# Performance work log

Measured on AMD Instinct MI355X. Metric: run time of the kernel, lower is better.

Reference implementation:

```python
import jax, jax.numpy as jnp
import numpy as np

V, E, H, W, L = 30000, 300, 512, 20, 512
EPS = 1e-8


def _lstm_dir(x, Wih, Whh):
    # x: [L, E]; PyTorch gate order i, f, g, o; bias=False
    Hh = Whh.shape[1]
    def step(carry, xt):
        h, c = carry
        g = Wih @ xt + Whh @ h
        i, f, gg, o = jnp.split(g, 4)
        c = jax.nn.sigmoid(f) * c + jax.nn.sigmoid(i) * jnp.tanh(gg)
        h = jax.nn.sigmoid(o) * jnp.tanh(c)
        return (h, c), h
    init = (jnp.zeros(Hh, x.dtype), jnp.zeros(Hh, x.dtype))
    _, hs = jax.lax.scan(step, init, x)
    return hs  # [L, H]


def _bilstm(x, Wih_f, Whh_f, Wih_b, Whh_b):
    hf = _lstm_dir(x, Wih_f, Whh_f)
    hb = _lstm_dir(x[::-1], Wih_b, Whh_b)[::-1]
    return jnp.concatenate([hf, hb], axis=-1)  # [L, 2H]


def _wcos_rows(a, b, w):
    # a,b: [L,H] (b may be broadcast of a single vector); w: [W,H] -> [L,W]
    A = a[:, None, :] * w[None]                       # [L,W,H]
    B = jnp.broadcast_to(b, a.shape)[:, None, :] * w[None]
    num = jnp.sum(A * B, axis=-1)
    na = jnp.maximum(jnp.linalg.norm(A, axis=-1), EPS)
    nb = jnp.maximum(jnp.linalg.norm(B, axis=-1), EPS)
    return num / (na * nb)


def _wcos_pair_max(a, b, w):
    # fused pairwise weighted cosine + max over q2: never builds [L1,L2,W,H]
    A = a[:, None, :] * w[None]                       # [L1,W,H]
    B = b[:, None, :] * w[None]                       # [L2,W,H]
    num = jnp.einsum('ikh,jkh->ijk', A, B)            # [L1,L2,W]
    na = jnp.maximum(jnp.linalg.norm(A, axis=-1), EPS)  # [L1,W]
    nb = jnp.maximum(jnp.linalg.norm(B, axis=-1), EPS)  # [L2,W]
    return jnp.max(num / (na[:, None, :] * nb[None, :, :]), axis=1)  # [L1,W]


def _cos_pair(a, b):
    num = a @ b.T                                     # [L1,L2]
    na = jnp.maximum(jnp.linalg.norm(a, axis=-1), EPS)
    nb = jnp.maximum(jnp.linalg.norm(b, axis=-1), EPS)
    return num / (na[:, None] * nb[None, :])


def _model(emb, q1_Wih_f, q1_Whh_f, q1_Wih_b, q1_Whh_b,
           q2_Wih_f, q2_Whh_f, q2_Wih_b, q2_Whh_b,
           W1, W2, W3, W4, W5, W6, q1_ids, q2_ids, l1, l2):
    Hh = W1.shape[1]
    x1 = emb[q1_ids[0, :l1]]                          # [L1,E]
    x2 = emb[q2_ids[0, :l2]]
    q1_outs = _bilstm(x1, q1_Wih_f, q1_Whh_f, q1_Wih_b, q1_Whh_b)
    q2_outs = _bilstm(x2, q2_Wih_f, q2_Whh_f, q2_Wih_b, q2_Whh_b)
    q1p, q1n = q1_outs[:, :Hh], q1_outs[:, Hh:]
    q2p, q2n = q2_outs[:, :Hh], q2_outs[:, Hh:]
    # full matching (vs q2 tail fwd / head bwd)
    m_pos_full = _wcos_rows(q1p, q2p[-1], W1)
    m_neg_full = _wcos_rows(q1n, q2n[0], W2)
    # max-pool matching over all q2 positions
    m_pos_max = _wcos_pair_max(q1p, q2p, W3)
    m_neg_max = _wcos_pair_max(q1n, q2n, W4)
    # attentive matching (cosine attention, mean-by-alpha)
    alpha_pos = _cos_pair(q1p, q2p)                   # [L1,L2]
    q2_pos_att = (alpha_pos @ q2p) / jnp.sum(alpha_pos, axis=1, keepdims=True)
    m_pos_atten = _wcos_rows(q1p, q2_pos_att, W5)
    alpha_neg = _cos_pair(q1n, q2n)
    q2_neg_att = (alpha_neg @ q2n) / jnp.sum(alpha_neg, axis=1, keepdims=True)
    m_neg_atten = _wcos_rows(q1n, q2_neg_att, W5)     # source uses W_5 here (not W_6), kept faithful
    return jnp.stack([m_pos_full, m_neg_full, m_pos_max,
                      m_neg_max, m_pos_atten, m_neg_atten])  # [6,L1,W]


def setup_inputs() -> dict:
    key = jax.random.key(0)
    ks = jax.random.split(key, 20)
    def n(k, shape, s=1.0):
        return jax.random.normal(k, shape, jnp.float32) * s
    return {
        'q1_inputs': jax.random.randint(ks[0], (1, L), 0, V),
        'q2_inputs': jax.random.randint(ks[1], (1, L), 0, V),
        'q1_lens': L,
        'q2_lens': L,
        'emb': n(ks[2], (V, E), 0.1),
        'q1_Wih_f': n(ks[3], (4 * H, E), 0.05), 'q1_Whh_f': n(ks[4], (4 * H, H), 0.05),
        'q1_Wih_b': n(ks[5], (4 * H, E), 0.05), 'q1_Whh_b': n(ks[6], (4 * H, H), 0.05),
        'q2_Wih_f': n(ks[7], (4 * H, E), 0.05), 'q2_Whh_f': n(ks[8], (4 * H, H), 0.05),
        'q2_Wih_b': n(ks[9], (4 * H, E), 0.05), 'q2_Whh_b': n(ks[10], (4 * H, H), 0.05),
        'W1': n(ks[11], (W, H)), 'W2': n(ks[12], (W, H)), 'W3': n(ks[13], (W, H)),
        'W4': n(ks[14], (W, H)), 'W5': n(ks[15], (W, H)), 'W6': n(ks[16], (W, H)),
    }


def reference(q1_inputs, q2_inputs, q1_lens, q2_lens, emb,
              q1_Wih_f, q1_Whh_f, q1_Wih_b, q1_Whh_b,
              q2_Wih_f, q2_Whh_f, q2_Wih_b, q2_Whh_b,
              W1, W2, W3, W4, W5, W6):
    return _model(emb, q1_Wih_f, q1_Whh_f, q1_Wih_b, q1_Whh_b,
                  q2_Wih_f, q2_Whh_f, q2_Wih_b, q2_Whh_b,
                  W1, W2, W3, W4, W5, W6,
                  q1_inputs, q2_inputs, q1_lens, q2_lens)
```

## Files before the change

kernel.cpp:

```cpp
#include <hip/hip_runtime.h>
#include <hip/hip_bf16.h>
#include <math.h>

#define LQ 512
#define HH 512
#define EE 300
#define WW 20
#define G4 2048
#define EPSF 1e-8f
#define RB 32
#define JPB 16

typedef __hip_bfloat16 bf16;
typedef unsigned long long u64;
typedef unsigned int u32;

__device__ __forceinline__ float fast_sigmoid(float x){
  x = fminf(fmaxf(x, -30.f), 30.f);
  return 1.f/(1.f + __expf(-x));
}
__device__ __forceinline__ float fast_tanh(float x){
  x = fminf(fmaxf(x, -15.f), 15.f);
  float e = __expf(2.f*x);
  return (e - 1.f)/(e + 1.f);
}

#define OFF_GIN   0
#define OFF_ALPHA 0
#define OFF_ATT   524288
#define OFF_NRM   1048576
#define OFF_NP    1089536
#define OFF_PMP   1179648
#define OFF_HS    (4*LQ*G4)
#define OFF_HPUB  (OFF_HS + 4*LQ*HH)
#define WS_NEEDED ((OFF_HPUB + 2*4*LQ*HH) * 4ULL)

__global__ __launch_bounds__(256) void k_sentinel(float* __restrict__ outp, float code)
{
  const int i = blockIdx.x*256 + threadIdx.x;
  if (i < 3072) outp[i] = code;
}

__global__ __launch_bounds__(256) void k_gather_gemm(
    const float* __restrict__ emb, const int* __restrict__ q1_ids, const int* __restrict__ q2_ids,
    const float* __restrict__ wih0, const float* __restrict__ wih1,
    const float* __restrict__ wih2, const float* __restrict__ wih3,
    float* __restrict__ gin)
{
  const int g = blockIdx.z;
  const int* ids = (g < 2) ? q1_ids : q2_ids;
  const float* wih = (g==0)?wih0:(g==1)?wih1:(g==2)?wih2:wih3;
  __shared__ __align__(16) float As[16][68];
  __shared__ __align__(16) float Bs[16][68];
  __shared__ int rowid[64];
  const int tid = threadIdx.x;
  const int tx = tid & 15, ty = tid >> 4;
  const int m0 = blockIdx.y*64, n0 = blockIdx.x*64;
  if (tid < 64) rowid[tid] = ids[m0 + tid];
  __syncthreads();
  float acc[4][4] = {};
  for (int k0 = 0; k0 < EE; k0 += 16) {
    for (int idx = tid; idx < 1024; idx += 256) {
      int r = idx >> 4, kk = idx & 15;
      int k = k0 + kk;
      As[kk][r] = (k < EE) ? emb[(size_t)rowid[r]*EE + k] : 0.f;
      Bs[kk][r] = (k < EE) ? wih[(size_t)(n0+r)*EE + k] : 0.f;
    }
    __syncthreads();
    #pragma unroll
    for (int kk=0;kk<16;kk++){
      float4 a = *reinterpret_cast<const float4*>(&As[kk][ty*4]);
      float4 b = *reinterpret_cast<const float4*>(&Bs[kk][tx*4]);
      acc[0][0]=fmaf(a.x,b.x,acc[0][0]); acc[0][1]=fmaf(a.x,b.y,acc[0][1]);
      acc[0][2]=fmaf(a.x,b.z,acc[0][2]); acc[0][3]=fmaf(a.x,b.w,acc[0][3]);
      acc[1][0]=fmaf(a.y,b.x,acc[1][0]); acc[1][1]=fmaf(a.y,b.y,acc[1][1]);
      acc[1][2]=fmaf(a.y,b.z,acc[1][2]); acc[1][3]=fmaf(a.y,b.w,acc[1][3]);
      acc[2][0]=fmaf(a.z,b.x,acc[2][0]); acc[2][1]=fmaf(a.z,b.y,acc[2][1]);
      acc[2][2]=fmaf(a.z,b.z,acc[2][2]); acc[2][3]=fmaf(a.z,b.w,acc[2][3]);
      acc[3][0]=fmaf(a.w,b.x,acc[3][0]); acc[3][1]=fmaf(a.w,b.y,acc[3][1]);
      acc[3][2]=fmaf(a.w,b.z,acc[3][2]); acc[3][3]=fmaf(a.w,b.w,acc[3][3]);
    }
    __syncthreads();
  }
  float* outp = gin + (size_t)g*LQ*G4;
  #pragma unroll
  for (int u=0;u<4;u++)
    #pragma unroll
    for (int v=0;v<4;v++)
      outp[(size_t)(m0+ty*4+u)*G4 + n0+tx*4+v] = acc[u][v];
}

__global__ __launch_bounds__(512)
__attribute__((amdgpu_waves_per_eu(1,2)))
void k_lstm(
    const float* __restrict__ whh0, const float* __restrict__ whh1,
    const float* __restrict__ whh2, const float* __restrict__ whh3,
    const float* __restrict__ gin, float* __restrict__ hs, u64* __restrict__ hpub)
{
  const int g = (blockIdx.x >> 1) & 3;
  const int b = ((blockIdx.x >> 3) << 1) | (blockIdx.x & 1);
  const float* whh = (g==0)?whh0:(g==1)?whh1:(g==2)?whh2:whh3;
  const int tid = threadIdx.x;
  const int row_local = tid >> 3;
  const int chunk = tid & 7;
  const int gate = row_local >> 4;
  const int jj = row_local & 15;
  const int grow = gate*HH + b*JPB + jj;
  const int rot = chunk;

  const float4* wv4 = reinterpret_cast<const float4*>(whh + (size_t)grow*HH + chunk*64);
  float4 w0  = wv4[(0  + rot) & 15];
  float4 w1  = wv4[(1  + rot) & 15];
  float4 w2  = wv4[(2  + rot) & 15];
  float4 w3  = wv4[(3  + rot) & 15];
  float4 w4  = wv4[(4  + rot) & 15];
  float4 w5  = wv4[(5  + rot) & 15];
  float4 w6  = wv4[(6  + rot) & 15];
  float4 w7  = wv4[(7  + rot) & 15];
  float4 w8  = wv4[(8  + rot) & 15];
  float4 w9  = wv4[(9  + rot) & 15];
  float4 w10 = wv4[(10 + rot) & 15];
  float4 w11 = wv4[(11 + rot) & 15];
  float4 w12 = wv4[(12 + rot) & 15];
  float4 w13 = wv4[(13 + rot) & 15];
  float4 w14 = wv4[(14 + rot) & 15];
  float4 w15 = wv4[(15 + rot) & 15];

  __shared__ __align__(16) float h_lds[HH];
  __shared__ float gdot[64];

  const float* ginp = gin + (size_t)g*LQ*G4;
  float* hsg = hs + (size_t)g*LQ*HH;
  u64* hpg = hpub + (size_t)g*LQ*HH;
  const bool fwd = ((g & 1) == 0);

  float pg_cur = 0.f, pg_nxt = 0.f, creg = 0.f;
  if (tid < 64) {
    const int sidx0 = fwd ? 0 : (LQ-1);
    pg_cur = ginp[(size_t)sidx0*G4 + (size_t)(tid>>4)*HH + b*JPB + (tid&15)];
  }

  for (int s=0; s<LQ; ++s) {
    const int sidx = fwd ? s : (LQ-1-s);
    if (s == 0) {
      h_lds[tid] = 0.f;
      __syncthreads();
    } else {
      const int hidx = fwd ? (s-1) : (LQ-s);
      const u64 want = (u64)(u32)(hidx + 1);
      const u64* hp = hpg + (size_t)hidx*HH + tid;
      u64 v = __hip_atomic_load(hp, __ATOMIC_RELAXED, __HIP_MEMORY_SCOPE_AGENT);
      while ((v >> 32) != want) {
        v = __hip_atomic_load(hp, __ATOMIC_RELAXED, __HIP_MEMORY_SCOPE_AGENT);
      }
      h_lds[tid] = __uint_as_float((u32)v);
      __syncthreads();
    }
    float p0=0.f, p1=0.f, p2=0.f, p3=0.f;
    {
      const float4* hld4 = reinterpret_cast<const float4*>(h_lds) + (chunk << 4);
      #define MSTEP(q, pp) { float4 hh = hld4[((q)+rot)&15]; \
        pp = fmaf(w##q.x, hh.x, pp); pp = fmaf(w##q.y, hh.y, pp); \
        pp = fmaf(w##q.z, hh.z, pp); pp = fmaf(w##q.w, hh.w, pp); }
      MSTEP(0,p0)  MSTEP(1,p1)  MSTEP(2,p2)  MSTEP(3,p3)
      MSTEP(4,p0)  MSTEP(5,p1)  MSTEP(6,p2)  MSTEP(7,p3)
      MSTEP(8,p0)  MSTEP(9,p1)  MSTEP(10,p2) MSTEP(11,p3)
      MSTEP(12,p0) MSTEP(13,p1) MSTEP(14,p2) MSTEP(15,p3)
      #undef MSTEP
    }
    if (tid < 64) {
      const int snx = (s+1 < LQ) ? (s+1) : s;
      const int sidxn = fwd ? snx : (LQ-1-snx);
      pg_nxt = ginp[(size_t)sidxn*G4 + (size_t)(tid>>4)*HH + b*JPB + (tid&15)];
    }
    float partial = (p0 + p1) + (p2 + p3);
    partial += __shfl_xor(partial, 1);
    partial += __shfl_xor(partial, 2);
    partial += __shfl_xor(partial, 4);
    if (chunk == 0) gdot[row_local] = partial;
    __syncthreads();
    if (tid < 64) {
      float x = gdot[tid] + pg_cur;
      const int gt = tid >> 4;
      float t = (gt == 2) ? 2.f*x : x;
      t = fminf(fmaxf(t, -30.f), 30.f);
      float sg = 1.f/(1.f + __expf(-t));
      float y = (gt == 2) ? 2.f*sg - 1.f : sg;
      float vf = __shfl_down(y, 16);
      float vg = __shfl_down(y, 32);
      float vo = __shfl_down(y, 48);
      if (tid < 16) {
        float c = vf*creg + y*vg;
        creg = c;
        float tc = fminf(fmaxf(2.f*c, -30.f), 30.f);
        float th = 2.f/(1.f + __expf(-tc)) - 1.f;
        float h = vo*th;
        const int j = b*JPB + tid;
        u64 pack = ((u64)(u32)(sidx + 1) << 32) | (u64)__float_as_uint(h);
        __hip_atomic_store(hpg + (size_t)sidx*HH + j, pack,
                           __ATOMIC_RELAXED, __HIP_MEMORY_SCOPE_AGENT);
        hsg[(size_t)sidx*HH + j] = h;
      }
      pg_cur = pg_nxt;
    }
  }
}

__global__ __launch_bounds__(256) void k_norms(
    const float* __restrict__ hs, const float* __restrict__ W3, const float* __restrict__ W4,
    float* __restrict__ nrm, float* __restrict__ np_)
{
  const int l = blockIdx.x;
  const int which = blockIdx.y;
  const int hsidx = (which==0)?0:(which==1)?2:(which==2)?1:3;
  const float* P = hs + (size_t)hsidx*LQ*HH + (size_t)l*HH;
  const float* Wt = (which < 2) ? W3 : W4;
  const int tid = threadIdx.x;
  const int w = tid >> 6, ln = tid & 63;
  __shared__ float p[HH];
  p[tid] = P[tid]; p[tid+256] = P[tid+256];
  __syncthreads();
  if (w == 0) {
    float v = 0.f;
    #pragma unroll
    for (int q=0;q<8;q++){ float x = p[ln+64*q]; v = fmaf(x,x,v); }
    #pragma unroll
    for (int o=32;o>0;o>>=1) v += __shfl_xor(v,o);
    if (ln==0) np_[which*LQ + l] = fmaxf(sqrtf(v), EPSF);
  }
  for (int k=w; k<WW; k+=4){
    const float* wk = Wt + (size_t)k*HH;
    float v = 0.f;
    #pragma unroll
    for (int q=0;q<8;q++){
      int e = ln + 64*q;
      float a = p[e]*wk[e];
      v = fmaf(a,a,v);
    }
    #pragma unroll
    for (int o=32;o>0;o>>=1) v += __shfl_xor(v,o);
    if (ln==0) nrm[(size_t)which*LQ*WW + (size_t)l*WW + k] = fmaxf(sqrtf(v), EPSF);
  }
}

__global__ __launch_bounds__(256) void k_alpha(
    const float* __restrict__ hs, const float* __restrict__ np_, float* __restrict__ alpha)
{
  const int z = blockIdx.z;
  const float* A = hs + (size_t)(z?1:0)*LQ*HH;
  const float* B = hs + (size_t)(z?3:2)*LQ*HH;
  const float* nai = np_ + (z?2:0)*LQ;
  const float* nbj = np_ + (z?3:1)*LQ;
  float* outp = alpha + (size_t)z*LQ*LQ;
  __shared__ __align__(16) float As[16][68], Bs[16][68];
  const int tid = threadIdx.x;
  const int tx = tid & 15, ty = tid >> 4;
  const int i0 = blockIdx.y*64, j0 = blockIdx.x*64;
  float acc[4][4] = {};
  for (int k0=0;k0<HH;k0+=16){
    for (int idx=tid; idx<1024; idx+=256){
      int r = idx>>4, kk = idx&15;
      As[kk][r] = A[(size_t)(i0+r)*HH + k0+kk];
      Bs[kk][r] = B[(size_t)(j0+r)*HH + k0+kk];
    }
    __syncthreads();
    #pragma unroll
    for (int kk=0;kk<16;kk++){
      float4 a = *reinterpret_cast<const float4*>(&As[kk][ty*4]);
      float4 b = *reinterpret_cast<const float4*>(&Bs[kk][tx*4]);
      acc[0][0]=fmaf(a.x,b.x,acc[0][0]); acc[0][1]=fmaf(a.x,b.y,acc[0][1]);
      acc[0][2]=fmaf(a.x,b.z,acc[0][2]); acc[0][3]=fmaf(a.x,b.w,acc[0][3]);
      acc[1][0]=fmaf(a.y,b.x,acc[1][0]); acc[1][1]=fmaf(a.y,b.y,acc[1][1]);
      acc[1][2]=fmaf(a.y,b.z,acc[1][2]); acc[1][3]=fmaf(a.y,b.w,acc[1][3]);
      acc[2][0]=fmaf(a.z,b.x,acc[2][0]); acc[2][1]=fmaf(a.z,b.y,acc[2][1]);
      acc[2][2]=fmaf(a.z,b.z,acc[2][2]); acc[2][3]=fmaf(a.z,b.w,acc[2][3]);
      acc[3][0]=fmaf(a.w,b.x,acc[3][0]); acc[3][1]=fmaf(a.w,b.y,acc[3][1]);
      acc[3][2]=fmaf(a.w,b.z,acc[3][2]); acc[3][3]=fmaf(a.w,b.w,acc[3][3]);
    }
    __syncthreads();
  }
  #pragma unroll
  for (int u=0;u<4;u++){
    float ina = 1.f/nai[i0+ty*4+u];
    #pragma unroll
    for (int v=0;v<4;v++)
      outp[(size_t)(i0+ty*4+u)*LQ + j0+tx*4+v] = acc[u][v]*ina/nbj[j0+tx*4+v];
  }
}

__global__ __launch_bounds__(256) void k_att(
    const float* __restrict__ alpha, const float* __restrict__ hs,
    float* __restrict__ att)
{
  const int z = blockIdx.z;
  const float* A = alpha + (size_t)z*LQ*LQ;
  const float* B = hs + (size_t)(z?3:2)*LQ*HH;
  float* outp = att + (size_t)z*LQ*HH;
  __shared__ __align__(16) float As[16][68], Bs[16][68];
  const int tid = threadIdx.x;
  const int tx = tid & 15, ty = tid >> 4;
  const int i0 = blockIdx.y*64, h0 = blockIdx.x*64;
  float acc[4][4] = {};
  float rsum[4] = {};
  for (int j0=0;j0<LQ;j0+=16){
    for (int idx=tid; idx<1024; idx+=256){
      int r = idx>>4, kk = idx&15;
      As[kk][r] = A[(size_t)(i0+r)*LQ + j0+kk];
    }
    for (int idx=tid; idx<1024; idx+=256){
      int jjr = idx>>6, hh = idx&63;
      Bs[jjr][hh] = B[(size_t)(j0+jjr)*HH + h0+hh];
    }
    __syncthreads();
    #pragma unroll
    for (int kk=0;kk<16;kk++){
      float4 a = *reinterpret_cast<const float4*>(&As[kk][ty*4]);
      float4 b = *reinterpret_cast<const float4*>(&Bs[kk][tx*4]);
      rsum[0]+=a.x; rsum[1]+=a.y; rsum[2]+=a.z; rsum[3]+=a.w;
      acc[0][0]=fmaf(a.x,b.x,acc[0][0]); acc[0][1]=fmaf(a.x,b.y,acc[0][1]);
      acc[0][2]=fmaf(a.x,b.z,acc[0][2]); acc[0][3]=fmaf(a.x,b.w,acc[0][3]);
      acc[1][0]=fmaf(a.y,b.x,acc[1][0]); acc[1][1]=fmaf(a.y,b.y,acc[1][1]);
      acc[1][2]=fmaf(a.y,b.z,acc[1][2]); acc[1][3]=fmaf(a.y,b.w,acc[1][3]);
      acc[2][0]=fmaf(a.z,b.x,acc[2][0]); acc[2][1]=fmaf(a.z,b.y,acc[2][1]);
      acc[2][2]=fmaf(a.z,b.z,acc[2][2]); acc[2][3]=fmaf(a.z,b.w,acc[2][3]);
      acc[3][0]=fmaf(a.w,b.x,acc[3][0]); acc[3][1]=fmaf(a.w,b.y,acc[3][1]);
      acc[3][2]=fmaf(a.w,b.z,acc[3][2]); acc[3][3]=fmaf(a.w,b.w,acc[3][3]);
    }
    __syncthreads();
  }
  #pragma unroll
  for (int u=0;u<4;u++){
    float inv = 1.f/rsum[u];
    #pragma unroll
    for (int v=0;v<4;v++)
      outp[(size_t)(i0+ty*4+u)*HH + h0+tx*4+v] = acc[u][v]*inv;
  }
}

__global__ __launch_bounds__(256) void k_wcos(
    const float* __restrict__ hs, const float* __restrict__ att,
    const float* __restrict__ W1, const float* __restrict__ W2, const float* __restrict__ W5,
    float* __restrict__ outp)
{
  const int l = blockIdx.x;
  const int which = blockIdx.y;
  const int tid = threadIdx.x;
  const float* a; const float* c; const float* Wt; int m;
  switch (which) {
    case 0:  a = hs + (size_t)0*LQ*HH + (size_t)l*HH; c = hs + (size_t)2*LQ*HH + (size_t)(LQ-1)*HH; Wt = W1; m = 0; break;
    case 1:  a = hs + (size_t)1*LQ*HH + (size_t)l*HH; c = hs + (size_t)3*LQ*HH;                     Wt = W2; m = 1; break;
    case 2:  a = hs + (size_t)0*LQ*HH + (size_t)l*HH; c = att + (size_t)0*LQ*HH + (size_t)l*HH;     Wt = W5; m = 4; break;
    default: a = hs + (size_t)1*LQ*HH + (size_t)l*HH; c = att + (size_t)1*LQ*HH + (size_t)l*HH;     Wt = W5; m = 5; break;
  }
  __shared__ float av[HH], cv[HH];
  const int w = tid >> 6, ln = tid & 63;
  av[tid]=a[tid]; av[tid+256]=a[tid+256];
  cv[tid]=c[tid]; cv[tid+256]=c[tid+256];
  __syncthreads();
  for (int k=w; k<WW; k+=4){
    const float* wk = Wt + (size_t)k*HH;
    float num=0.f, na=0.f, nc=0.f;
    #pragma unroll
    for (int q=0;q<8;q++){
      int e = ln + 64*q;
      float w1 = wk[e];
      float aw = av[e]*w1;
      float cw = cv[e]*w1;
      num = fmaf(aw,cw,num);
      na  = fmaf(aw,aw,na);
      nc  = fmaf(cw,cw,nc);
    }
    #pragma unroll
    for (int o=32;o>0;o>>=1){
      num += __shfl_xor(num,o);
      na  += __shfl_xor(na,o);
      nc  += __shfl_xor(nc,o);
    }
    if (ln==0){
      float d = fmaxf(sqrtf(na),EPSF)*fmaxf(sqrtf(nc),EPSF);
      outp[((size_t)m*LQ + l)*WW + k] = num/d;
    }
  }
}

__global__ __launch_bounds__(256) void k_pairmax(
    const float* __restrict__ hs, const float* __restrict__ W3, const float* __restrict__ W4,
    const float* __restrict__ nrm, float* __restrict__ pm_part)
{
  const int it = blockIdx.x;
  const int jt = blockIdx.y;
  const int z  = blockIdx.z;
  const int mm = z >> 1, kh = z & 1;
  const int k0 = kh*10;
  const float* A = hs + (size_t)(mm?1:0)*LQ*HH;
  const float* B = hs + (size_t)(mm?3:2)*LQ*HH;
  const float* Wt = mm ? W4 : W3;
  const float* nb = nrm + (size_t)(mm?3:1)*LQ*WW;
  const int tid = threadIdx.x;
  const int tx = tid & 31;
  const int ty = tid >> 5;
  const int i0 = it*64;
  const int j  = jt*32 + tx;

  __shared__ __align__(16) float As[64][128];
  __shared__ __align__(16) float Bs[32][132];
  __shared__ __align__(16) float Ws[10][128];

  float acc[8][10];
  #pragma unroll
  for (int r=0;r<8;r++)
    #pragma unroll
    for (int q=0;q<10;q++) acc[r][q]=0.f;

  for (int hc=0; hc<4; ++hc){
    const int hbase = hc*128;
    for (int idx=tid; idx<2048; idx+=256){
      int row = idx >> 5, c4 = idx & 31;
      *reinterpret_cast<float4*>(&As[row][c4*4]) =
        *reinterpret_cast<const float4*>(&A[(size_t)(i0+row)*HH + hbase + c4*4]);
    }
    for (int idx=tid; idx<1024; idx+=256){
      int row = idx >> 5, c4 = idx & 31;
      *reinterpret_cast<float4*>(&Bs[row][c4*4]) =
        *reinterpret_cast<const float4*>(&B[(size_t)(jt*32+row)*HH + hbase + c4*4]);
    }
    for (int idx=tid; idx<1280; idx+=256){
      int kk = idx >> 7, cc = idx & 127;
      float wv = Wt[(size_t)(k0+kk)*HH + hbase + cc];
      Ws[kk][cc] = wv*wv;
    }
    __syncthreads();
    #pragma unroll 2
    for (int h4=0; h4<32; ++h4){
      float4 b = *reinterpret_cast<const float4*>(&Bs[tx][h4*4]);
      float4 sa[8];
      #pragma unroll
      for (int r=0;r<8;r++){
        float4 a = *reinterpret_cast<const float4*>(&As[ty*8+r][h4*4]);
        sa[r].x = a.x*b.x; sa[r].y = a.y*b.y;
        sa[r].z = a.z*b.z; sa[r].w = a.w*b.w;
      }
      #pragma unroll
      for (int q=0;q<10;q++){
        float4 w = *reinterpret_cast<const float4*>(&Ws[q][h4*4]);
        #pragma unroll
        for (int r=0;r<8;r++){
          acc[r][q] = fmaf(sa[r].x, w.x, acc[r][q]);
          acc[r][q] = fmaf(sa[r].y, w.y, acc[r][q]);
          acc[r][q] = fmaf(sa[r].z, w.z, acc[r][q]);
          acc[r][q] = fmaf(sa[r].w, w.w, acc[r][q]);
        }
      }
    }
    __syncthreads();
  }

  float nbv[10];
  #pragma unroll
  for (int q=0;q<10;q++) nbv[q] = 1.f / nb[(size_t)j*WW + k0 + q];
  #pragma unroll
  for (int r=0;r<8;r++){
    #pragma unroll
    for (int q=0;q<10;q++){
      float v = acc[r][q] * nbv[q];
      #pragma unroll
      for (int o=1;o<32;o<<=1) v = fmaxf(v, __shfl_xor(v, o, 32));
      if (tx==0)
        pm_part[((((size_t)z*8 + it)*16 + jt)*64 + (ty*8+r))*10 + q] = v;
    }
  }
}

__global__ __launch_bounds__(256) void k_pmfin(
    const float* __restrict__ pm_part, const float* __restrict__ nrm,
    float* __restrict__ outp)
{
  const int idx = blockIdx.x*256 + threadIdx.x;
  if (idx >= 2*LQ*WW) return;
  const int mm = idx / (LQ*WW);
  const int rem = idx - mm*LQ*WW;
  const int i = rem / WW, k = rem % WW;
  const int it = i >> 6, il = i & 63;
  const int kh = k / 10, kl = k % 10;
  const int z = mm*2 + kh;
  float v = -3.4e38f;
  #pragma unroll
  for (int jt=0; jt<16; ++jt)
    v = fmaxf(v, pm_part[((((size_t)z*8 + it)*16 + jt)*64 + il)*10 + kl]);
  const float* na = nrm + (size_t)(mm?2:0)*LQ*WW;
  outp[((size_t)(mm+2)*LQ + i)*WW + k] = v / na[(size_t)i*WW + k];
}

extern "C" void kernel_launch(void* const* d_in, const int* in_sizes, int n_in,
                              void* d_out, int out_size, void* d_ws, size_t ws_size,
                              hipStream_t stream)
{
  float* outp = (float*)d_out;

  float code = 0.f;
  if (n_in != 19)                    code = 101.f;
  else if (in_sizes[0]  != 512)      code = 102.f;
  else if (in_sizes[4]  != 9000000)  code = 104.f;
  else if (in_sizes[6]  != 1048576)  code = 106.f;
  else if (out_size     != 61440)    code = 108.f;
  else if (ws_size      < WS_NEEDED) code = 109.f;
  if (code != 0.f) {
    k_sentinel<<<12, 256, 0, stream>>>(outp, code);
    return;
  }

  const int* q1_ids = (const int*)d_in[0];
  const int* q2_ids = (const int*)d_in[1];
  const float* emb      = (const float*)d_in[4];
  const float* q1_wih_f = (const float*)d_in[5];
  const float* q1_whh_f = (const float*)d_in[6];
  const float* q1_wih_b = (const float*)d_in[7];
  const float* q1_whh_b = (const float*)d_in[8];
  const float* q2_wih_f = (const float*)d_in[9];
  const float* q2_whh_f = (const float*)d_in[10];
  const float* q2_wih_b = (const float*)d_in[11];
  const float* q2_whh_b = (const float*)d_in[12];
  const float* W1 = (const float*)d_in[13];
  const float* W2 = (const float*)d_in[14];
  const float* W3 = (const float*)d_in[15];
  const float* W4 = (const float*)d_in[16];
  const float* W5 = (const float*)d_in[17];
  float* ws = (float*)d_ws;

  float* gin   = ws + OFF_GIN;
  float* hsv   = ws + OFF_HS;
  u64*   hpub  = (u64*)(ws + OFF_HPUB);
  float* alpha = ws + OFF_ALPHA;
  float* att   = ws + OFF_ATT;
  float* nrm   = ws + OFF_NRM;
  float* np_   = ws + OFF_NP;
  float* pmp   = ws + OFF_PMP;

  k_gather_gemm<<<dim3(32,8,4), 256, 0, stream>>>(emb, q1_ids, q2_ids,
      q1_wih_f, q1_wih_b, q2_wih_f, q2_wih_b, gin);
  k_lstm<<<dim3(4*RB), 512, 0, stream>>>(q1_whh_f, q1_whh_b, q2_whh_f, q2_whh_b,
      gin, hsv, hpub);
  k_norms<<<dim3(LQ,4), 256, 0, stream>>>(hsv, W3, W4, nrm, np_);
  k_alpha<<<dim3(8,8,2), 256, 0, stream>>>(hsv, np_, alpha);
  k_att<<<dim3(8,8,2), 256, 0, stream>>>(alpha, hsv, att);
  k_wcos<<<dim3(LQ,4), 256, 0, stream>>>(hsv, att, W1, W2, W5, outp);
  k_pairmax<<<dim3(8,16,4), 256, 0, stream>>>(hsv, W3, W4, nrm, pmp);
  k_pmfin<<<dim3(80), 256, 0, stream>>>(pmp, nrm, outp);
}
```

Measured before the change: 1.225 ms.

## Fuse input-projection GEMM into LSTM kernel with tile-ready flags for overlap

Merges the gather+input-GEMM and the persistent LSTM recurrence into one launch. Extra blocks compute 128x128 GEMM tiles and publish a magic tag per tile, and LSTM blocks spin on the tag covering the timesteps they are about to consume. This lets the recurrence start before the whole projection finishes and drops a kernel boundary. The GEMM tile is also enlarged to 128x128 with vectorized stores. Tags are never reset, so a stale TAG_MAGIC from a previous call could let LSTM blocks read gin before it is rewritten. The design also relies on all 384 blocks being co-resident to avoid deadlock.

Result: slower. 1.515 ms (+23.7%).

```diff
diff --git a/kernel.cpp b/kernel.cpp
--- a/kernel.cpp
+++ b/kernel.cpp
@@ -10,20 +10,11 @@
 #define EPSF 1e-8f
 #define RB 32
 #define JPB 16
+#define TAG_MAGIC 0x7E57A11Bu
 
 typedef __hip_bfloat16 bf16;
 typedef unsigned long long u64;
 typedef unsigned int u32;
-
-__device__ __forceinline__ float fast_sigmoid(float x){
-  x = fminf(fmaxf(x, -30.f), 30.f);
-  return 1.f/(1.f + __expf(-x));
-}
-__device__ __forceinline__ float fast_tanh(float x){
-  x = fminf(fmaxf(x, -15.f), 15.f);
-  float e = __expf(2.f*x);
-  return (e - 1.f)/(e + 1.f);
-}
 
 #define OFF_GIN   0
 #define OFF_ALPHA 0
@@ -33,7 +24,13 @@
 #define OFF_PMP   1179648
 #define OFF_HS    (4*LQ*G4)
 #define OFF_HPUB  (OFF_HS + 4*LQ*HH)
-#define WS_NEEDED ((OFF_HPUB + 2*4*LQ*HH) * 4ULL)
+#define OFF_TAG   (OFF_HPUB + 2*4*LQ*HH)
+#define WS_NEEDED ((OFF_TAG + 1024) * 4ULL)
+
+__device__ __forceinline__ float load_f32_agent(const float* p){
+  u32 v = __hip_atomic_load((const u32*)p, __ATOMIC_RELAXED, __HIP_MEMORY_SCOPE_AGENT);
+  return __uint_as_float(v);
+}
 
 __global__ __launch_bounds__(256) void k_sentinel(float* __restrict__ outp, float code)
 {
@@ -41,72 +38,83 @@
   if (i < 3072) outp[i] = code;
 }
 
-__global__ __launch_bounds__(256) void k_gather_gemm(
+__global__ __launch_bounds__(512)
+__attribute__((amdgpu_waves_per_eu(1,2)))
+void k_fusedgl(
     const float* __restrict__ emb, const int* __restrict__ q1_ids, const int* __restrict__ q2_ids,
     const float* __restrict__ wih0, const float* __restrict__ wih1,
     const float* __restrict__ wih2, const float* __restrict__ wih3,
-    float* __restrict__ gin)
-{
-  const int g = blockIdx.z;
-  const int* ids = (g < 2) ? q1_ids : q2_ids;
-  const float* wih = (g==0)?wih0:(g==1)?wih1:(g==2)?wih2:wih3;
-  __shared__ __align__(16) float As[16][68];
-  __shared__ __align__(16) float Bs[16][68];
-  __shared__ int rowid[64];
-  const int tid = threadIdx.x;
-  const int tx = tid & 15, ty = tid >> 4;
-  const int m0 = blockIdx.y*64, n0 = blockIdx.x*64;
-  if (tid < 64) rowid[tid] = ids[m0 + tid];
-  __syncthreads();
-  float acc[4][4] = {};
-  for (int k0 = 0; k0 < EE; k0 += 16) {
-    for (int idx = tid; idx < 1024; idx += 256) {
-      int r = idx >> 4, kk = idx & 15;
-      int k = k0 + kk;
-      As[kk][r] = (k < EE) ? emb[(size_t)rowid[r]*EE + k] : 0.f;
-      Bs[kk][r] = (k < EE) ? wih[(size_t)(n0+r)*EE + k] : 0.f;
-    }
-    __syncthreads();
-    #pragma unroll
-    for (int kk=0;kk<16;kk++){
-      float4 a = *reinterpret_cast<const float4*>(&As[kk][ty*4]);
-      float4 b = *reinterpret_cast<const float4*>(&Bs[kk][tx*4]);
-      acc[0][0]=fmaf(a.x,b.x,acc[0][0]); acc[0][1]=fmaf(a.x,b.y,acc[0][1]);
-      acc[0][2]=fmaf(a.x,b.z,acc[0][2]); acc[0][3]=fmaf(a.x,b.w,acc[0][3]);
-      acc[1][0]=fmaf(a.y,b.x,acc[1][0]); acc[1][1]=fmaf(a.y,b.y,acc[1][1]);
-      acc[1][2]=fmaf(a.y,b.z,acc[1][2]); acc[1][3]=fmaf(a.y,b.w,acc[1][3]);
-      acc[2][0]=fmaf(a.z,b.x,acc[2][0]); acc[2][1]=fmaf(a.z,b.y,acc[2][1]);
-      acc[2][2]=fmaf(a.z,b.z,acc[2][2]); acc[2][3]=fmaf(a.z,b.w,acc[2][3]);
-      acc[3][0]=fmaf(a.w,b.x,acc[3][0]); acc[3][1]=fmaf(a.w,b.y,acc[3][1]);
-      acc[3][2]=fmaf(a.w,b.z,acc[3][2]); acc[3][3]=fmaf(a.w,b.w,acc[3][3]);
-    }
-    __syncthreads();
-  }
-  float* outp = gin + (size_t)g*LQ*G4;
-  #pragma unroll
-  for (int u=0;u<4;u++)
-    #pragma unroll
-    for (int v=0;v<4;v++)
-      outp[(size_t)(m0+ty*4+u)*G4 + n0+tx*4+v] = acc[u][v];
-}
-
-__global__ __launch_bounds__(512)
-__attribute__((amdgpu_waves_per_eu(1,2)))
-void k_lstm(
     const float* __restrict__ whh0, const float* __restrict__ whh1,
     const float* __restrict__ whh2, const float* __restrict__ whh3,
-    const float* __restrict__ gin, float* __restrict__ hs, u64* __restrict__ hpub)
-{
+    float* __restrict__ gin, float* __restrict__ hs, u64* __restrict__ hpub,
+    u32* __restrict__ tags)
+{
+  __shared__ __align__(16) float As[16][132];
+  __shared__ __align__(16) float Bs[16][132];
+  __shared__ int rowid[128];
+  __shared__ __align__(16) float h_lds[HH];
+  __shared__ float gdot[64];
+  const int tid = threadIdx.x;
+
+  if (blockIdx.x >= 128) {
+    const int gi = blockIdx.x - 128;
+    const int g2 = gi & 3, mt = (gi >> 2) & 3, nt = gi >> 4;
+    const int* ids = (g2 < 2) ? q1_ids : q2_ids;
+    const float* wih = (g2==0)?wih0:(g2==1)?wih1:(g2==2)?wih2:wih3;
+    const int m0 = mt*128, n0 = nt*128;
+    if (tid < 128) rowid[tid] = ids[m0 + tid];
+    __syncthreads();
+    const int tx = tid & 15, ty = tid >> 4;
+    float acc[4][8] = {};
+    for (int k0 = 0; k0 < EE; k0 += 16) {
+      for (int idx = tid; idx < 2048; idx += 512) {
+        int r = idx >> 4, kk = idx & 15;
+        int k = k0 + kk;
+        As[kk][r] = (k < EE) ? emb[(size_t)rowid[r]*EE + k] : 0.f;
+        Bs[kk][r] = (k < EE) ? wih[(size_t)(n0+r)*EE + k] : 0.f;
+      }
+      __syncthreads();
+      #pragma unroll
+      for (int kk=0;kk<16;kk++){
+        float4 a  = *reinterpret_cast<const float4*>(&As[kk][ty*4]);
+        float4 b0 = *reinterpret_cast<const float4*>(&Bs[kk][tx*8]);
+        float4 b1 = *reinterpret_cast<const float4*>(&Bs[kk][tx*8+4]);
+        #define FMA8(u, av) \
+          acc[u][0]=fmaf(av,b0.x,acc[u][0]); acc[u][1]=fmaf(av,b0.y,acc[u][1]); \
+          acc[u][2]=fmaf(av,b0.z,acc[u][2]); acc[u][3]=fmaf(av,b0.w,acc[u][3]); \
+          acc[u][4]=fmaf(av,b1.x,acc[u][4]); acc[u][5]=fmaf(av,b1.y,acc[u][5]); \
+          acc[u][6]=fmaf(av,b1.z,acc[u][6]); acc[u][7]=fmaf(av,b1.w,acc[u][7]);
+        FMA8(0, a.x) FMA8(1, a.y) FMA8(2, a.z) FMA8(3, a.w)
+        #undef FMA8
+      }
+      __syncthreads();
+    }
+    float* og = gin + (size_t)g2*LQ*G4;
+    #pragma unroll
+    for (int u=0;u<4;u++){
+      float4 lo = make_float4(acc[u][0],acc[u][1],acc[u][2],acc[u][3]);
+      float4 hi = make_float4(acc[u][4],acc[u][5],acc[u][6],acc[u][7]);
+      *reinterpret_cast<float4*>(&og[(size_t)(m0+ty*4+u)*G4 + n0+tx*8])   = lo;
+      *reinterpret_cast<float4*>(&og[(size_t)(m0+ty*4+u)*G4 + n0+tx*8+4]) = hi;
+    }
+    __threadfence();
+    __syncthreads();
+    if (tid == 0)
+      __hip_atomic_store(&tags[(g2*4+mt)*16+nt], TAG_MAGIC,
+                         __ATOMIC_RELEASE, __HIP_MEMORY_SCOPE_AGENT);
+    return;
+  }
+
   const int g = (blockIdx.x >> 1) & 3;
   const int b = ((blockIdx.x >> 3) << 1) | (blockIdx.x & 1);
   const float* whh = (g==0)?whh0:(g==1)?whh1:(g==2)?whh2:whh3;
-  const int tid = threadIdx.x;
   const int row_local = tid >> 3;
   const int chunk = tid & 7;
   const int gate = row_local >> 4;
   const int jj = row_local & 15;
   const int grow = gate*HH + b*JPB + jj;
   const int rot = chunk;
+  const int nt0 = b >> 3;
 
   const float4* wv4 = reinterpret_cast<const float4*>(whh + (size_t)grow*HH + chunk*64);
   float4 w0  = wv4[(0  + rot) & 15];
@@ -126,18 +134,26 @@
   float4 w14 = wv4[(14 + rot) & 15];
   float4 w15 = wv4[(15 + rot) & 15];
 
-  __shared__ __align__(16) float h_lds[HH];
-  __shared__ float gdot[64];
-
   const float* ginp = gin + (size_t)g*LQ*G4;
   float* hsg = hs + (size_t)g*LQ*HH;
   u64* hpg = hpub + (size_t)g*LQ*HH;
   const bool fwd = ((g & 1) == 0);
 
+  #define WAIT_TILE(mt_) { \
+    if (tid < 64) { \
+      const int gt_ = tid >> 4; \
+      const u32* tp_ = tags + ((g*4 + (mt_))*16) + gt_*4 + nt0; \
+      while (__hip_atomic_load(tp_, __ATOMIC_ACQUIRE, __HIP_MEMORY_SCOPE_AGENT) != TAG_MAGIC) {} \
+    } \
+    __syncthreads(); \
+  }
+
   float pg_cur = 0.f, pg_nxt = 0.f, creg = 0.f;
-  if (tid < 64) {
+  {
     const int sidx0 = fwd ? 0 : (LQ-1);
-    pg_cur = ginp[(size_t)sidx0*G4 + (size_t)(tid>>4)*HH + b*JPB + (tid&15)];
+    WAIT_TILE(sidx0 >> 7);
+    if (tid < 64)
+      pg_cur = load_f32_agent(&ginp[(size_t)sidx0*G4 + (size_t)(tid>>4)*HH + b*JPB + (tid&15)]);
   }
 
   for (int s=0; s<LQ; ++s) {
@@ -168,10 +184,11 @@
       MSTEP(12,p0) MSTEP(13,p1) MSTEP(14,p2) MSTEP(15,p3)
       #undef MSTEP
     }
+    const int snx = (s+1 < LQ) ? (s+1) : s;
+    const int sidxn = fwd ? snx : (LQ-1-snx);
+    if ((sidxn >> 7) != (sidx >> 7)) WAIT_TILE(sidxn >> 7);
     if (tid < 64) {
-      const int snx = (s+1 < LQ) ? (s+1) : s;
-      const int sidxn = fwd ? snx : (LQ-1-snx);
-      pg_nxt = ginp[(size_t)sidxn*G4 + (size_t)(tid>>4)*HH + b*JPB + (tid&15)];
+      pg_nxt = load_f32_agent(&ginp[(size_t)sidxn*G4 + (size_t)(tid>>4)*HH + b*JPB + (tid&15)]);
     }
     float partial = (p0 + p1) + (p2 + p3);
     partial += __shfl_xor(partial, 1);
@@ -204,6 +221,7 @@
       pg_cur = pg_nxt;
     }
   }
+  #undef WAIT_TILE
 }
 
 __global__ __launch_bounds__(256) void k_norms(
@@ -534,12 +552,13 @@
   float* att   = ws + OFF_ATT;
   float* nrm   = ws + OFF_NRM;
   float* np_   = ws + OFF_NP;
+  u32*   tags  = (u32*)(ws + OFF_TAG);
   float* pmp   = ws + OFF_PMP;
 
-  k_gather_gemm<<<dim3(32,8,4), 256, 0, stream>>>(emb, q1_ids, q2_ids,
-      q1_wih_f, q1_wih_b, q2_wih_f, q2_wih_b, gin);
-  k_lstm<<<dim3(4*RB), 512, 0, stream>>>(q1_whh_f, q1_whh_b, q2_whh_f, q2_whh_b,
-      gin, hsv, hpub);
+  k_fusedgl<<<dim3(384), 512, 0, stream>>>(emb, q1_ids, q2_ids,
+      q1_wih_f, q1_wih_b, q2_wih_f, q2_wih_b,
+      q1_whh_f, q1_whh_b, q2_whh_f, q2_whh_b,
+      gin, hsv, hpub, tags);
   k_norms<<<dim3(LQ,4), 256, 0, stream>>>(hsv, W3, W4, nrm, np_);
   k_alpha<<<dim3(8,8,2), 256, 0, stream>>>(hsv, np_, alpha);
   k_att<<<dim3(8,8,2), 256, 0, stream>>>(alpha, hsv, att);
```
